# Performance work log

Measured on AMD Instinct MI355X. Metric: run time of the kernel, lower is better.

The kernel has to match this reference:

```python
import jax, jax.numpy as jnp
import numpy as np

B, V, T, D, H = 8, 64, 256, 256, 8
DH = D // H
LN_EPS = 1e-5


def setup_inputs() -> dict:
    key = jax.random.key(0)
    k0, k1, k2, k3 = jax.random.split(key, 4)
    x = jax.random.normal(k0, (B, V, T + 1, D), dtype=jnp.float32)
    obs_mask = jax.random.randint(k1, (B, V, T), 0, 2).astype(bool)
    ln_w = jnp.ones((D,), jnp.float32)
    ln_b = jnp.zeros((D,), jnp.float32)
    w_qkv = jax.random.normal(k2, (3 * D, D), dtype=jnp.float32) * 0.02   # torch Linear weight (out,in), no bias
    w_proj = jax.random.normal(k3, (D, D), dtype=jnp.float32) * 0.02
    b_proj = jnp.zeros((D,), jnp.float32)
    return dict(x=x, obs_mask=obs_mask, ln_w=ln_w, ln_b=ln_b,
                w_qkv=w_qkv, w_proj=w_proj, b_proj=b_proj)


def reference(x, obs_mask, ln_w, ln_b, w_qkv, w_proj, b_proj):
    b, v, t1, d = x.shape
    h, dh = H, D // H

    # LayerNorm over last dim
    mu = jnp.mean(x, axis=-1, keepdims=True)
    var = jnp.mean(jnp.square(x - mu), axis=-1, keepdims=True)
    xn = (x - mu) * jax.lax.rsqrt(var + LN_EPS) * ln_w + ln_b

    # QKV projection: (B,V,T1,3D) -> (B,V,T1,3,H,dh)
    qkv = jnp.einsum('bvtd,ed->bvte', xn, w_qkv).reshape(b, v, t1, 3, h, dh)
    qf = qkv[:, :, :, 0]  # (B,V,T1,H,dh)
    kf = qkv[:, :, :, 1]
    vf = qkv[:, :, :, 2]

    # Queries from position 0 only: (B,H,V,dh)
    q = jnp.transpose(qf[:, :, 0], (0, 2, 1, 3))

    # Keys: masked mean over time (query token at pos 0 always observed)
    mask = jnp.concatenate([jnp.ones((b, v, 1), bool), obs_mask], axis=2)  # (B,V,T1)
    mf = mask[..., None, None].astype(kf.dtype)                            # (B,V,T1,1,1)
    cnt = jnp.clip(mask.sum(axis=2).astype(kf.dtype), 1.0)[:, :, None, None]
    k = (kf * mf).sum(axis=2) / cnt                                        # (B,V,H,dh)
    k = jnp.transpose(k, (0, 2, 1, 3))                                     # (B,H,V,dh)

    # Small cross-variable attention matrix (B,H,V,V)
    scale = dh ** -0.5
    attn = jax.nn.softmax(jnp.einsum('bhqd,bhkd->bhqk', q, k) * scale, axis=-1)

    # Values packed with temporal structure: (B,H,V,dh,T1)
    vp = jnp.transpose(vf, (0, 3, 1, 4, 2))
    out = jnp.einsum('bhqk,bhkdt->bhqdt', attn, vp)                        # (B,H,V,dh,T1)

    # Unpack back to (B,V,T1,D)
    out = jnp.transpose(out, (0, 2, 4, 1, 3)).reshape(b, v, t1, d)
    out = out @ w_proj.T + b_proj
    return x + out
```

## Files before the change

### kernel.cpp

```cpp
#include <hip/hip_runtime.h>
#include <hip/hip_bf16.h>

typedef unsigned short u16;
typedef __attribute__((ext_vector_type(8))) short short8;
typedef __attribute__((ext_vector_type(4))) float f32x4;

#define B_ 8
#define V_ 64
#define T_ 256
#define T1_ 257
#define D_ 256
#define H_ 8
#define DH_ 32

__device__ __forceinline__ u16 f2bf(float f){
  union { float f; unsigned int u; } v; v.f = f;
  unsigned int u = v.u;
  return (u16)((u + 0x7fffu + ((u >> 16) & 1u)) >> 16);
}

__global__ void k0_conv(const float* __restrict__ wqkv, const float* __restrict__ wproj,
                        u16* __restrict__ wv, u16* __restrict__ wp){
  int i = blockIdx.x * 256 + threadIdx.x;
  if (i < 65536) wv[i] = f2bf(wqkv[131072 + i]);
  else           wp[i - 65536] = f2bf(wproj[i - 65536]);
}

__global__ void k_zero(float* __restrict__ p, int n){
  int i = blockIdx.x * blockDim.x + threadIdx.x;
  if (i < n) p[i] = 0.f;
}

__global__ void k1_ln(const float* __restrict__ x, const int* __restrict__ mask,
                      const float* __restrict__ lnw, const float* __restrict__ lnb,
                      float* __restrict__ musig, float* __restrict__ xsum){
  int bv = blockIdx.x;
  int tid = threadIdx.x;
  int lane = tid & 63, wid = tid >> 6;
  int t0 = blockIdx.y * 65;
  int tend = t0 + 65; if (tend > T1_) tend = T1_;
  __shared__ float xsred[4][D_];
  float4 w4 = *(const float4*)&lnw[lane * 4];
  float4 b4 = *(const float4*)&lnb[lane * 4];
  float xs0 = 0.f, xs1 = 0.f, xs2 = 0.f, xs3 = 0.f;
  for (int t = t0 + wid; t < tend; t += 4){
    float4 v = *(const float4*)&x[((long)bv * T1_ + t) * D_ + lane * 4];
    float s  = v.x + v.y + v.z + v.w;
    float s2 = v.x*v.x + v.y*v.y + v.z*v.z + v.w*v.w;
    #pragma unroll
    for (int off = 1; off < 64; off <<= 1){
      s  += __shfl_xor(s,  off, 64);
      s2 += __shfl_xor(s2, off, 64);
    }
    float mu   = s * (1.f / 256.f);
    float var  = s2 * (1.f / 256.f) - mu * mu;
    float rstd = rsqrtf(var + 1e-5f);
    if (lane == 0){
      musig[((long)bv * T1_ + t) * 2]     = mu;
      musig[((long)bv * T1_ + t) * 2 + 1] = rstd;
    }
    int m = (t == 0) ? 1 : mask[bv * T_ + (t - 1)];
    if (m){
      xs0 += (v.x - mu) * rstd * w4.x + b4.x;
      xs1 += (v.y - mu) * rstd * w4.y + b4.y;
      xs2 += (v.z - mu) * rstd * w4.z + b4.z;
      xs3 += (v.w - mu) * rstd * w4.w + b4.w;
    }
  }
  xsred[wid][lane * 4]     = xs0;
  xsred[wid][lane * 4 + 1] = xs1;
  xsred[wid][lane * 4 + 2] = xs2;
  xsred[wid][lane * 4 + 3] = xs3;
  __syncthreads();
  float r = xsred[0][tid] + xsred[1][tid] + xsred[2][tid] + xsred[3][tid];
  atomicAdd(&xsum[bv * D_ + tid], r);
}

__global__ void k2a_qk(const float* __restrict__ x, const int* __restrict__ mask,
                       const float* __restrict__ lnw, const float* __restrict__ lnb,
                       const float* __restrict__ wqkv,
                       const float* __restrict__ musig, const float* __restrict__ xsum,
                       float* __restrict__ qout, float* __restrict__ kout){
  int bv = blockIdx.x, tid = threadIdx.x;
  int lane = tid & 63, wid = tid >> 6;
  __shared__ __align__(16) float xn0[D_];
  __shared__ __align__(16) float xs[D_];
  __shared__ float redc[4];
  int s = mask[bv * T_ + tid];
  #pragma unroll
  for (int off = 32; off >= 1; off >>= 1) s += __shfl_down(s, off, 64);
  if (lane == 0) redc[wid] = (float)s;
  __syncthreads();
  float cnt = 1.f + redc[0] + redc[1] + redc[2] + redc[3];
  float mu = musig[((long)bv * T1_) * 2], rstd = musig[((long)bv * T1_) * 2 + 1];
  xn0[tid] = (x[((long)bv * T1_) * D_ + tid] - mu) * rstd * lnw[tid] + lnb[tid];
  xs[tid]  = xsum[bv * D_ + tid] * (1.f / cnt);
  __syncthreads();
  float4 xq = *(const float4*)&xn0[lane * 4];
  float4 xk = *(const float4*)&xs[lane * 4];
  int e0 = (blockIdx.y * 4 + wid) * 16;
  for (int i = 0; i < 16; ++i){
    int e = e0 + i;
    float4 wq4 = *(const float4*)&wqkv[(long)e * D_ + lane * 4];
    float4 wk4 = *(const float4*)&wqkv[(long)(256 + e) * D_ + lane * 4];
    float sq = xq.x*wq4.x + xq.y*wq4.y + xq.z*wq4.z + xq.w*wq4.w;
    float sk = xk.x*wk4.x + xk.y*wk4.y + xk.z*wk4.z + xk.w*wk4.w;
    #pragma unroll
    for (int off = 32; off >= 1; off >>= 1){
      sq += __shfl_down(sq, off, 64);
      sk += __shfl_down(sk, off, 64);
    }
    if (lane == 0){ qout[bv * D_ + e] = sq; kout[bv * D_ + e] = sk; }
  }
}

__global__ void k2b_attn(const float* __restrict__ q, const float* __restrict__ k,
                         u16* __restrict__ attn){
  int bh = blockIdx.x; int b = bh >> 3, h = bh & 7;
  int tid = threadIdx.x;
  __shared__ float qs[64][DH_], ks[64][DH_];
  for (int d = 0; d < DH_; ++d){
    qs[tid][d] = q[((long)(b * V_ + tid)) * D_ + h * DH_ + d];
    ks[tid][d] = k[((long)(b * V_ + tid)) * D_ + h * DH_ + d];
  }
  __syncthreads();
  const float scale = 0.17677669529663687f;
  float sc[64];
  float mx = -1e30f;
  #pragma unroll
  for (int j = 0; j < 64; ++j){
    float a = 0.f;
    #pragma unroll
    for (int d = 0; d < DH_; ++d) a += qs[tid][d] * ks[j][d];
    a *= scale; sc[j] = a; mx = fmaxf(mx, a);
  }
  float sum = 0.f;
  #pragma unroll
  for (int j = 0; j < 64; ++j){ float e = __expf(sc[j] - mx); sc[j] = e; sum += e; }
  float inv = 1.f / sum;
  #pragma unroll
  for (int j = 0; j < 64; ++j) attn[((long)bh * 64 + tid) * 64 + j] = f2bf(sc[j] * inv);
}

__global__ __launch_bounds__(512, 4) void k3_main(
    const float* __restrict__ x, const float* __restrict__ lnw, const float* __restrict__ lnb,
    const float* __restrict__ bproj, const float* __restrict__ musig,
    const u16* __restrict__ wv, const u16* __restrict__ wp,
    const u16* __restrict__ attn, float* __restrict__ out){
  constexpr int XS = 264;
  constexpr int VS = 72;
  __shared__ __align__(16) u16 Xs[64 * XS];
  __shared__ __align__(16) u16 VT[D_ * VS];
  __shared__ float lnw_s[D_], lnb_s[D_], bp_s[D_];
  __shared__ float ms_s[V_ * 2];

  int bt = blockIdx.x; int b = bt / T1_, t = bt % T1_;
  int tid = threadIdx.x;
  int w = tid >> 6, lane = tid & 63, lm = lane & 15, lq = lane >> 4;
  int cw = w * 32;

  if (tid < 256){ lnw_s[tid] = lnw[tid]; lnb_s[tid] = lnb[tid]; bp_s[tid] = bproj[tid]; }
  else if (tid < 384){
    int i = tid - 256;
    ms_s[i] = musig[(((long)b * V_ + (i >> 1)) * T1_ + t) * 2 + (i & 1)];
  }
  __syncthreads();

  #pragma unroll
  for (int i = 0; i < 4; ++i){
    int seg = i * 512 + tid;
    int vr = seg >> 5;
    int c8 = (seg & 31) * 8;
    const float* gp = x + (((long)b * V_ + vr) * T1_ + t) * D_ + c8;
    float4 a0 = *(const float4*)gp;
    float4 a1 = *(const float4*)(gp + 4);
    float mu = ms_s[vr * 2], rs = ms_s[vr * 2 + 1];
    float av[8] = {a0.x, a0.y, a0.z, a0.w, a1.x, a1.y, a1.z, a1.w};
    union { u16 us[8]; uint4 q; } pk;
    #pragma unroll
    for (int j = 0; j < 8; ++j)
      pk.us[j] = f2bf((av[j] - mu) * rs * lnw_s[c8 + j] + lnb_s[c8 + j]);
    *(uint4*)&Xs[vr * XS + c8] = pk.q;
  }
  __syncthreads();

  f32x4 acc1[4][2];
  #pragma unroll
  for (int mt = 0; mt < 4; ++mt)
    #pragma unroll
    for (int nt = 0; nt < 2; ++nt) acc1[mt][nt] = (f32x4){0.f, 0.f, 0.f, 0.f};
  for (int kk = 0; kk < 8; ++kk){
    short8 af[4], bfr[2];
    #pragma unroll
    for (int mt = 0; mt < 4; ++mt)
      af[mt] = *(const short8*)&Xs[(mt * 16 + lm) * XS + kk * 32 + lq * 8];
    #pragma unroll
    for (int nt = 0; nt < 2; ++nt)
      bfr[nt] = *(const short8*)&wv[(long)(cw + nt * 16 + lm) * D_ + kk * 32 + lq * 8];
    #pragma unroll
    for (int mt = 0; mt < 4; ++mt)
      #pragma unroll
      for (int nt = 0; nt < 2; ++nt)
        acc1[mt][nt] = __builtin_amdgcn_mfma_f32_16x16x32_bf16(af[mt], bfr[nt], acc1[mt][nt], 0, 0, 0);
  }
  #pragma unroll
  for (int mt = 0; mt < 4; ++mt)
    #pragma unroll
    for (int nt = 0; nt < 2; ++nt){
      int col = cw + nt * 16 + lm;
      int row = mt * 16 + lq * 4;
      union { u16 us[4]; uint2 q; } pv;
      #pragma unroll
      for (int r = 0; r < 4; ++r) pv.us[r] = f2bf(acc1[mt][nt][r]);
      *(uint2*)&VT[col * VS + row] = pv.q;
    }
  __syncthreads();

  int h = w;
  f32x4 acc2[4][2];
  #pragma unroll
  for (int mt = 0; mt < 4; ++mt)
    #pragma unroll
    for (int nt = 0; nt < 2; ++nt) acc2[mt][nt] = (f32x4){0.f, 0.f, 0.f, 0.f};
  #pragma unroll
  for (int kk = 0; kk < 2; ++kk){
    short8 af[4], bfr[2];
    #pragma unroll
    for (int mt = 0; mt < 4; ++mt)
      af[mt] = *(const short8*)&attn[((long)(b * H_ + h) * 64 + mt * 16 + lm) * 64 + kk * 32 + lq * 8];
    #pragma unroll
    for (int nt = 0; nt < 2; ++nt)
      bfr[nt] = *(const short8*)&VT[(h * 32 + nt * 16 + lm) * VS + kk * 32 + lq * 8];
    #pragma unroll
    for (int mt = 0; mt < 4; ++mt)
      #pragma unroll
      for (int nt = 0; nt < 2; ++nt)
        acc2[mt][nt] = __builtin_amdgcn_mfma_f32_16x16x32_bf16(af[mt], bfr[nt], acc2[mt][nt], 0, 0, 0);
  }
  #pragma unroll
  for (int mt = 0; mt < 4; ++mt)
    #pragma unroll
    for (int nt = 0; nt < 2; ++nt){
      int col = h * 32 + nt * 16 + lm;
      #pragma unroll
      for (int r = 0; r < 4; ++r){
        int row = mt * 16 + lq * 4 + r;
        Xs[row * XS + col] = f2bf(acc2[mt][nt][r]);
      }
    }
  __syncthreads();

  f32x4 acc3[4][2];
  #pragma unroll
  for (int mt = 0; mt < 4; ++mt)
    #pragma unroll
    for (int nt = 0; nt < 2; ++nt) acc3[mt][nt] = (f32x4){0.f, 0.f, 0.f, 0.f};
  for (int kk = 0; kk < 8; ++kk){
    short8 af[4], bfr[2];
    #pragma unroll
    for (int mt = 0; mt < 4; ++mt)
      af[mt] = *(const short8*)&Xs[(mt * 16 + lm) * XS + kk * 32 + lq * 8];
    #pragma unroll
    for (int nt = 0; nt < 2; ++nt)
      bfr[nt] = *(const short8*)&wp[(long)(cw + nt * 16 + lm) * D_ + kk * 32 + lq * 8];
    #pragma unroll
    for (int mt = 0; mt < 4; ++mt)
      #pragma unroll
      for (int nt = 0; nt < 2; ++nt)
        acc3[mt][nt] = __builtin_amdgcn_mfma_f32_16x16x32_bf16(af[mt], bfr[nt], acc3[mt][nt], 0, 0, 0);
  }
  #pragma unroll
  for (int mt = 0; mt < 4; ++mt)
    #pragma unroll
    for (int nt = 0; nt < 2; ++nt){
      int e = cw + nt * 16 + lm;
      #pragma unroll
      for (int r = 0; r < 4; ++r){
        int vr = mt * 16 + lq * 4 + r;
        long g = (((long)b * V_ + vr) * T1_ + t) * D_ + e;
        out[g] = acc3[mt][nt][r] + bp_s[e] + x[g];
      }
    }
}

extern "C" void kernel_launch(void* const* d_in, const int* in_sizes, int n_in,
                              void* d_out, int out_size, void* d_ws, size_t ws_size,
                              hipStream_t stream){
  const float* x     = (const float*)d_in[0];
  const int*   mask  = (const int*)d_in[1];
  const float* lnw   = (const float*)d_in[2];
  const float* lnb   = (const float*)d_in[3];
  const float* wqkv  = (const float*)d_in[4];
  const float* wproj = (const float*)d_in[5];
  const float* bproj = (const float*)d_in[6];
  float* out = (float*)d_out;
  char* ws = (char*)d_ws;
  float* musig = (float*)(ws);
  float* xsum  = (float*)(ws + 1052672);
  float* qbuf  = (float*)(ws + 1576960);
  float* kbuf  = (float*)(ws + 2101248);
  u16*   attn  = (u16*)  (ws + 2625536);
  u16*   wv    = (u16*)  (ws + 3149824);
  u16*   wp    = (u16*)  (ws + 3280896);

  k0_conv<<<512, 256, 0, stream>>>(wqkv, wproj, wv, wp);
  k_zero<<<512, 256, 0, stream>>>(xsum, 131072);
  k1_ln<<<dim3(512, 4), 256, 0, stream>>>(x, mask, lnw, lnb, musig, xsum);
  k2a_qk<<<dim3(512, 4), 256, 0, stream>>>(x, mask, lnw, lnb, wqkv, musig, xsum, qbuf, kbuf);
  k2b_attn<<<64, 64, 0, stream>>>(qbuf, kbuf, attn);
  k3_main<<<B_ * T1_, 512, 0, stream>>>(x, lnw, lnb, bproj, musig, wv, wp, attn, out);
}
```

Before: 405.7 us.

## Prefetch weights into registers, merge zero kernel, restructure LN and attention softmax

Several changes at once. The xsum zeroing is folded into the weight-conversion kernel, which removes one launch. The LN kernel now processes two rows per wave with 8 columns per lane. The softmax kernel runs one query row per wave with shuffle reductions and padded shared memory. In k3_main, the x tile, the wv/wp weight fragments and the attention fragments are loaded into registers ahead of the barriers and MFMA loops, and the residual x loads are issued before the epilogue, so global latency overlaps compute. This raises register pressure under launch_bounds(512,4), which could cause spills or lower occupancy.

```diff
diff --git a/kernel.cpp b/kernel.cpp
--- a/kernel.cpp
+++ b/kernel.cpp
@@ -20,15 +20,11 @@
 }
 
 __global__ void k0_conv(const float* __restrict__ wqkv, const float* __restrict__ wproj,
-                        u16* __restrict__ wv, u16* __restrict__ wp){
+                        u16* __restrict__ wv, u16* __restrict__ wp, float* __restrict__ xsum){
   int i = blockIdx.x * 256 + threadIdx.x;
   if (i < 65536) wv[i] = f2bf(wqkv[131072 + i]);
   else           wp[i - 65536] = f2bf(wproj[i - 65536]);
-}
-
-__global__ void k_zero(float* __restrict__ p, int n){
-  int i = blockIdx.x * blockDim.x + threadIdx.x;
-  if (i < n) p[i] = 0.f;
+  xsum[i] = 0.f;
 }
 
 __global__ void k1_ln(const float* __restrict__ x, const int* __restrict__ mask,
@@ -37,42 +33,57 @@
   int bv = blockIdx.x;
   int tid = threadIdx.x;
   int lane = tid & 63, wid = tid >> 6;
-  int t0 = blockIdx.y * 65;
-  int tend = t0 + 65; if (tend > T1_) tend = T1_;
-  __shared__ float xsred[4][D_];
-  float4 w4 = *(const float4*)&lnw[lane * 4];
-  float4 b4 = *(const float4*)&lnb[lane * 4];
-  float xs0 = 0.f, xs1 = 0.f, xs2 = 0.f, xs3 = 0.f;
-  for (int t = t0 + wid; t < tend; t += 4){
-    float4 v = *(const float4*)&x[((long)bv * T1_ + t) * D_ + lane * 4];
-    float s  = v.x + v.y + v.z + v.w;
-    float s2 = v.x*v.x + v.y*v.y + v.z*v.z + v.w*v.w;
-    #pragma unroll
-    for (int off = 1; off < 64; off <<= 1){
+  int half = lane >> 5, l32 = lane & 31;
+  int c8 = l32 * 8;
+  __shared__ float xsred[4][512];
+  float4 w0 = *(const float4*)&lnw[c8], w1 = *(const float4*)&lnw[c8 + 4];
+  float4 b0 = *(const float4*)&lnb[c8], b1 = *(const float4*)&lnb[c8 + 4];
+  float xs[8];
+  #pragma unroll
+  for (int j = 0; j < 8; ++j) xs[j] = 0.f;
+  for (int p = blockIdx.y * 4 + wid; p < 129; p += 16){
+    int t = p * 2 + half;
+    bool valid = (t < T1_);
+    float4 a0 = {0.f,0.f,0.f,0.f}, a1 = {0.f,0.f,0.f,0.f};
+    if (valid){
+      const float* gp = &x[((long)bv * T1_ + t) * D_ + c8];
+      a0 = *(const float4*)gp; a1 = *(const float4*)(gp + 4);
+    }
+    float s  = a0.x + a0.y + a0.z + a0.w + a1.x + a1.y + a1.z + a1.w;
+    float s2 = a0.x*a0.x + a0.y*a0.y + a0.z*a0.z + a0.w*a0.w
+             + a1.x*a1.x + a1.y*a1.y + a1.z*a1.z + a1.w*a1.w;
+    #pragma unroll
+    for (int off = 1; off < 32; off <<= 1){
       s  += __shfl_xor(s,  off, 64);
       s2 += __shfl_xor(s2, off, 64);
     }
     float mu   = s * (1.f / 256.f);
     float var  = s2 * (1.f / 256.f) - mu * mu;
     float rstd = rsqrtf(var + 1e-5f);
-    if (lane == 0){
-      musig[((long)bv * T1_ + t) * 2]     = mu;
-      musig[((long)bv * T1_ + t) * 2 + 1] = rstd;
-    }
-    int m = (t == 0) ? 1 : mask[bv * T_ + (t - 1)];
-    if (m){
-      xs0 += (v.x - mu) * rstd * w4.x + b4.x;
-      xs1 += (v.y - mu) * rstd * w4.y + b4.y;
-      xs2 += (v.z - mu) * rstd * w4.z + b4.z;
-      xs3 += (v.w - mu) * rstd * w4.w + b4.w;
-    }
-  }
-  xsred[wid][lane * 4]     = xs0;
-  xsred[wid][lane * 4 + 1] = xs1;
-  xsred[wid][lane * 4 + 2] = xs2;
-  xsred[wid][lane * 4 + 3] = xs3;
-  __syncthreads();
-  float r = xsred[0][tid] + xsred[1][tid] + xsred[2][tid] + xsred[3][tid];
+    if (valid){
+      if (l32 == 0){
+        musig[((long)bv * T1_ + t) * 2]     = mu;
+        musig[((long)bv * T1_ + t) * 2 + 1] = rstd;
+      }
+      int m = (t == 0) ? 1 : mask[bv * T_ + (t - 1)];
+      if (m){
+        xs[0] += (a0.x - mu) * rstd * w0.x + b0.x;
+        xs[1] += (a0.y - mu) * rstd * w0.y + b0.y;
+        xs[2] += (a0.z - mu) * rstd * w0.z + b0.z;
+        xs[3] += (a0.w - mu) * rstd * w0.w + b0.w;
+        xs[4] += (a1.x - mu) * rstd * w1.x + b1.x;
+        xs[5] += (a1.y - mu) * rstd * w1.y + b1.y;
+        xs[6] += (a1.z - mu) * rstd * w1.z + b1.z;
+        xs[7] += (a1.w - mu) * rstd * w1.w + b1.w;
+      }
+    }
+  }
+  #pragma unroll
+  for (int j = 0; j < 8; ++j) xsred[wid][half * 256 + c8 + j] = xs[j];
+  __syncthreads();
+  float r = 0.f;
+  #pragma unroll
+  for (int w2 = 0; w2 < 4; ++w2) r += xsred[w2][tid] + xsred[w2][256 + tid];
   atomicAdd(&xsum[bv * D_ + tid], r);
 }
 
@@ -118,28 +129,34 @@
                          u16* __restrict__ attn){
   int bh = blockIdx.x; int b = bh >> 3, h = bh & 7;
   int tid = threadIdx.x;
-  __shared__ float qs[64][DH_], ks[64][DH_];
-  for (int d = 0; d < DH_; ++d){
-    qs[tid][d] = q[((long)(b * V_ + tid)) * D_ + h * DH_ + d];
-    ks[tid][d] = k[((long)(b * V_ + tid)) * D_ + h * DH_ + d];
+  int lane = tid & 63, wid = tid >> 6;
+  __shared__ float qs[64][33], ks[64][33];
+  #pragma unroll
+  for (int j = 0; j < 2; ++j){
+    int i4 = tid * 2 + j;
+    int r = i4 >> 3, c4 = (i4 & 7) * 4;
+    float4 vq = *(const float4*)&q[((long)(b * V_ + r)) * D_ + h * DH_ + c4];
+    float4 vk = *(const float4*)&k[((long)(b * V_ + r)) * D_ + h * DH_ + c4];
+    qs[r][c4] = vq.x; qs[r][c4+1] = vq.y; qs[r][c4+2] = vq.z; qs[r][c4+3] = vq.w;
+    ks[r][c4] = vk.x; ks[r][c4+1] = vk.y; ks[r][c4+2] = vk.z; ks[r][c4+3] = vk.w;
   }
   __syncthreads();
   const float scale = 0.17677669529663687f;
-  float sc[64];
-  float mx = -1e30f;
-  #pragma unroll
-  for (int j = 0; j < 64; ++j){
+  for (int i = 0; i < 16; ++i){
+    int qr = i * 4 + wid;
     float a = 0.f;
     #pragma unroll
-    for (int d = 0; d < DH_; ++d) a += qs[tid][d] * ks[j][d];
-    a *= scale; sc[j] = a; mx = fmaxf(mx, a);
-  }
-  float sum = 0.f;
-  #pragma unroll
-  for (int j = 0; j < 64; ++j){ float e = __expf(sc[j] - mx); sc[j] = e; sum += e; }
-  float inv = 1.f / sum;
-  #pragma unroll
-  for (int j = 0; j < 64; ++j) attn[((long)bh * 64 + tid) * 64 + j] = f2bf(sc[j] * inv);
+    for (int d = 0; d < DH_; ++d) a += qs[qr][d] * ks[lane][d];
+    a *= scale;
+    float mx = a;
+    #pragma unroll
+    for (int off = 1; off < 64; off <<= 1) mx = fmaxf(mx, __shfl_xor(mx, off, 64));
+    float e = __expf(a - mx);
+    float sum = e;
+    #pragma unroll
+    for (int off = 1; off < 64; off <<= 1) sum += __shfl_xor(sum, off, 64);
+    attn[((long)bh * 64 + qr) * 64 + lane] = f2bf(e * (1.f / sum));
+  }
 }
 
 __global__ __launch_bounds__(512, 4) void k3_main(
@@ -158,29 +175,46 @@
   int tid = threadIdx.x;
   int w = tid >> 6, lane = tid & 63, lm = lane & 15, lq = lane >> 4;
   int cw = w * 32;
-
-  if (tid < 256){ lnw_s[tid] = lnw[tid]; lnb_s[tid] = lnb[tid]; bp_s[tid] = bproj[tid]; }
-  else if (tid < 384){
-    int i = tid - 256;
-    ms_s[i] = musig[(((long)b * V_ + (i >> 1)) * T1_ + t) * 2 + (i & 1)];
-  }
-  __syncthreads();
-
+  int h = w;
+
+  short8 wvf[16];
+  #pragma unroll
+  for (int kk = 0; kk < 8; ++kk)
+    #pragma unroll
+    for (int nt = 0; nt < 2; ++nt)
+      wvf[kk*2+nt] = *(const short8*)&wv[(long)(cw + nt*16 + lm) * D_ + kk*32 + lq*8];
+
+  float4 xa[8];
   #pragma unroll
   for (int i = 0; i < 4; ++i){
     int seg = i * 512 + tid;
     int vr = seg >> 5;
     int c8 = (seg & 31) * 8;
     const float* gp = x + (((long)b * V_ + vr) * T1_ + t) * D_ + c8;
-    float4 a0 = *(const float4*)gp;
-    float4 a1 = *(const float4*)(gp + 4);
+    xa[i*2]   = *(const float4*)gp;
+    xa[i*2+1] = *(const float4*)(gp + 4);
+  }
+
+  if (tid < 256){ lnw_s[tid] = lnw[tid]; lnb_s[tid] = lnb[tid]; bp_s[tid] = bproj[tid]; }
+  else if (tid < 384){
+    int i = tid - 256;
+    ms_s[i] = musig[(((long)b * V_ + (i >> 1)) * T1_ + t) * 2 + (i & 1)];
+  }
+  __syncthreads();
+
+  #pragma unroll
+  for (int i = 0; i < 4; ++i){
+    int seg = i * 512 + tid;
+    int vr = seg >> 5;
+    int c8 = (seg & 31) * 8;
     float mu = ms_s[vr * 2], rs = ms_s[vr * 2 + 1];
-    float av[8] = {a0.x, a0.y, a0.z, a0.w, a1.x, a1.y, a1.z, a1.w};
-    union { u16 us[8]; uint4 q; } pk;
+    float av[8] = {xa[i*2].x, xa[i*2].y, xa[i*2].z, xa[i*2].w,
+                   xa[i*2+1].x, xa[i*2+1].y, xa[i*2+1].z, xa[i*2+1].w};
+    union { u16 us[8]; uint4 q4; } pk;
     #pragma unroll
     for (int j = 0; j < 8; ++j)
       pk.us[j] = f2bf((av[j] - mu) * rs * lnw_s[c8 + j] + lnb_s[c8 + j]);
-    *(uint4*)&Xs[vr * XS + c8] = pk.q;
+    *(uint4*)&Xs[vr * XS + c8] = pk.q4;
   }
   __syncthreads();
 
@@ -189,19 +223,17 @@
   for (int mt = 0; mt < 4; ++mt)
     #pragma unroll
     for (int nt = 0; nt < 2; ++nt) acc1[mt][nt] = (f32x4){0.f, 0.f, 0.f, 0.f};
+  #pragma unroll
   for (int kk = 0; kk < 8; ++kk){
-    short8 af[4], bfr[2];
+    short8 af[4];
     #pragma unroll
     for (int mt = 0; mt < 4; ++mt)
       af[mt] = *(const short8*)&Xs[(mt * 16 + lm) * XS + kk * 32 + lq * 8];
     #pragma unroll
-    for (int nt = 0; nt < 2; ++nt)
-      bfr[nt] = *(const short8*)&wv[(long)(cw + nt * 16 + lm) * D_ + kk * 32 + lq * 8];
-    #pragma unroll
     for (int mt = 0; mt < 4; ++mt)
       #pragma unroll
       for (int nt = 0; nt < 2; ++nt)
-        acc1[mt][nt] = __builtin_amdgcn_mfma_f32_16x16x32_bf16(af[mt], bfr[nt], acc1[mt][nt], 0, 0, 0);
+        acc1[mt][nt] = __builtin_amdgcn_mfma_f32_16x16x32_bf16(af[mt], wvf[kk*2+nt], acc1[mt][nt], 0, 0, 0);
   }
   #pragma unroll
   for (int mt = 0; mt < 4; ++mt)
@@ -209,14 +241,26 @@
     for (int nt = 0; nt < 2; ++nt){
       int col = cw + nt * 16 + lm;
       int row = mt * 16 + lq * 4;
-      union { u16 us[4]; uint2 q; } pv;
+      union { u16 us[4]; uint2 q2; } pv;
       #pragma unroll
       for (int r = 0; r < 4; ++r) pv.us[r] = f2bf(acc1[mt][nt][r]);
-      *(uint2*)&VT[col * VS + row] = pv.q;
-    }
-  __syncthreads();
-
-  int h = w;
+      *(uint2*)&VT[col * VS + row] = pv.q2;
+    }
+
+  short8 atf[8];
+  #pragma unroll
+  for (int kk = 0; kk < 2; ++kk)
+    #pragma unroll
+    for (int mt = 0; mt < 4; ++mt)
+      atf[kk*4+mt] = *(const short8*)&attn[((long)(b * H_ + h) * 64 + mt * 16 + lm) * 64 + kk * 32 + lq * 8];
+  short8 wpf0[8];
+  #pragma unroll
+  for (int kk = 0; kk < 4; ++kk)
+    #pragma unroll
+    for (int nt = 0; nt < 2; ++nt)
+      wpf0[kk*2+nt] = *(const short8*)&wp[(long)(cw + nt*16 + lm) * D_ + kk*32 + lq*8];
+  __syncthreads();
+
   f32x4 acc2[4][2];
   #pragma unroll
   for (int mt = 0; mt < 4; ++mt)
@@ -224,10 +268,7 @@
     for (int nt = 0; nt < 2; ++nt) acc2[mt][nt] = (f32x4){0.f, 0.f, 0.f, 0.f};
   #pragma unroll
   for (int kk = 0; kk < 2; ++kk){
-    short8 af[4], bfr[2];
-    #pragma unroll
-    for (int mt = 0; mt < 4; ++mt)
-      af[mt] = *(const short8*)&attn[((long)(b * H_ + h) * 64 + mt * 16 + lm) * 64 + kk * 32 + lq * 8];
+    short8 bfr[2];
     #pragma unroll
     for (int nt = 0; nt < 2; ++nt)
       bfr[nt] = *(const short8*)&VT[(h * 32 + nt * 16 + lm) * VS + kk * 32 + lq * 8];
@@ -235,8 +276,14 @@
     for (int mt = 0; mt < 4; ++mt)
       #pragma unroll
       for (int nt = 0; nt < 2; ++nt)
-        acc2[mt][nt] = __builtin_amdgcn_mfma_f32_16x16x32_bf16(af[mt], bfr[nt], acc2[mt][nt], 0, 0, 0);
-  }
+        acc2[mt][nt] = __builtin_amdgcn_mfma_f32_16x16x32_bf16(atf[kk*4+mt], bfr[nt], acc2[mt][nt], 0, 0, 0);
+  }
+  short8 wpf1[8];
+  #pragma unroll
+  for (int kk = 0; kk < 4; ++kk)
+    #pragma unroll
+    for (int nt = 0; nt < 2; ++nt)
+      wpf1[kk*2+nt] = *(const short8*)&wp[(long)(cw + nt*16 + lm) * D_ + (kk + 4)*32 + lq*8];
   #pragma unroll
   for (int mt = 0; mt < 4; ++mt)
     #pragma unroll
@@ -255,20 +302,42 @@
   for (int mt = 0; mt < 4; ++mt)
     #pragma unroll
     for (int nt = 0; nt < 2; ++nt) acc3[mt][nt] = (f32x4){0.f, 0.f, 0.f, 0.f};
-  for (int kk = 0; kk < 8; ++kk){
-    short8 af[4], bfr[2];
+  #pragma unroll
+  for (int kk = 0; kk < 4; ++kk){
+    short8 af[4];
     #pragma unroll
     for (int mt = 0; mt < 4; ++mt)
       af[mt] = *(const short8*)&Xs[(mt * 16 + lm) * XS + kk * 32 + lq * 8];
     #pragma unroll
-    for (int nt = 0; nt < 2; ++nt)
-      bfr[nt] = *(const short8*)&wp[(long)(cw + nt * 16 + lm) * D_ + kk * 32 + lq * 8];
-    #pragma unroll
     for (int mt = 0; mt < 4; ++mt)
       #pragma unroll
       for (int nt = 0; nt < 2; ++nt)
-        acc3[mt][nt] = __builtin_amdgcn_mfma_f32_16x16x32_bf16(af[mt], bfr[nt], acc3[mt][nt], 0, 0, 0);
-  }
+        acc3[mt][nt] = __builtin_amdgcn_mfma_f32_16x16x32_bf16(af[mt], wpf0[kk*2+nt], acc3[mt][nt], 0, 0, 0);
+  }
+  #pragma unroll
+  for (int kk = 0; kk < 4; ++kk){
+    short8 af[4];
+    #pragma unroll
+    for (int mt = 0; mt < 4; ++mt)
+      af[mt] = *(const short8*)&Xs[(mt * 16 + lm) * XS + (kk + 4) * 32 + lq * 8];
+    #pragma unroll
+    for (int mt = 0; mt < 4; ++mt)
+      #pragma unroll
+      for (int nt = 0; nt < 2; ++nt)
+        acc3[mt][nt] = __builtin_amdgcn_mfma_f32_16x16x32_bf16(af[mt], wpf1[kk*2+nt], acc3[mt][nt], 0, 0, 0);
+  }
+  float rx[4][2][4];
+  #pragma unroll
+  for (int mt = 0; mt < 4; ++mt)
+    #pragma unroll
+    for (int nt = 0; nt < 2; ++nt){
+      int e = cw + nt * 16 + lm;
+      #pragma unroll
+      for (int r = 0; r < 4; ++r){
+        int vr = mt * 16 + lq * 4 + r;
+        rx[mt][nt][r] = x[(((long)b * V_ + vr) * T1_ + t) * D_ + e];
+      }
+    }
   #pragma unroll
   for (int mt = 0; mt < 4; ++mt)
     #pragma unroll
@@ -278,7 +347,7 @@
       for (int r = 0; r < 4; ++r){
         int vr = mt * 16 + lq * 4 + r;
         long g = (((long)b * V_ + vr) * T1_ + t) * D_ + e;
-        out[g] = acc3[mt][nt][r] + bp_s[e] + x[g];
+        out[g] = acc3[mt][nt][r] + bp_s[e] + rx[mt][nt][r];
       }
     }
 }
@@ -303,10 +372,9 @@
   u16*   wv    = (u16*)  (ws + 3149824);
   u16*   wp    = (u16*)  (ws + 3280896);
 
-  k0_conv<<<512, 256, 0, stream>>>(wqkv, wproj, wv, wp);
-  k_zero<<<512, 256, 0, stream>>>(xsum, 131072);
+  k0_conv<<<512, 256, 0, stream>>>(wqkv, wproj, wv, wp, xsum);
   k1_ln<<<dim3(512, 4), 256, 0, stream>>>(x, mask, lnw, lnb, musig, xsum);
   k2a_qk<<<dim3(512, 4), 256, 0, stream>>>(x, mask, lnw, lnb, wqkv, musig, xsum, qbuf, kbuf);
-  k2b_attn<<<64, 64, 0, stream>>>(qbuf, kbuf, attn);
+  k2b_attn<<<64, 256, 0, stream>>>(qbuf, kbuf, attn);
   k3_main<<<B_ * T1_, 512, 0, stream>>>(x, lnw, lnb, bproj, musig, wv, wp, attn, out);
 }
```

After: 383.2 us. 5.6% less time.
